# Kernel optimization log

Hardware: AMD Instinct MI355X
Metric: run time of the kernel (lower is better)

## Reference

```python
import jax, jax.numpy as jnp
import numpy as np

B, N, SEQ_LEN, OUT_LEN, E = 4, 5000, 128, 128, 80000
C_IN = SEQ_LEN + OUT_LEN  # DConv input is concat([X, H])


def setup_inputs() -> dict:
    key = jax.random.key(0)
    ks = jax.random.split(key, 9)
    scale = 0.02
    return {
        "x": jax.random.normal(ks[0], (B, N, SEQ_LEN), dtype=jnp.float32),
        "edge_index": jax.random.randint(ks[1], (2, E), 0, N, dtype=jnp.int32),
        "edge_weight": jax.random.uniform(ks[2], (E,), dtype=jnp.float32),
        "Wz": scale * jax.random.normal(ks[3], (2, 2, C_IN, OUT_LEN), dtype=jnp.float32),
        "bz": jnp.zeros((OUT_LEN,), jnp.float32),
        "Wr": scale * jax.random.normal(ks[4], (2, 2, C_IN, OUT_LEN), dtype=jnp.float32),
        "br": jnp.zeros((OUT_LEN,), jnp.float32),
        "Wh": scale * jax.random.normal(ks[5], (2, 2, C_IN, OUT_LEN), dtype=jnp.float32),
        "bh": jnp.zeros((OUT_LEN,), jnp.float32),
    }


def reference(x, edge_index, edge_weight, Wz, bz, Wr, br, Wh, bh):
    src, dst = edge_index[0], edge_index[1]
    # weighted out-/in-degrees and random-walk normalization (safe reciprocal)
    deg_out = jax.ops.segment_sum(edge_weight, src, num_segments=N)
    deg_in = jax.ops.segment_sum(edge_weight, dst, num_segments=N)
    dinv_out = jnp.where(deg_out > 0, 1.0 / deg_out, 0.0)
    dinv_in = jnp.where(deg_in > 0, 1.0 / deg_in, 0.0)
    coef_o = edge_weight * dinv_out[src]  # D_out^-1 W, per-edge
    coef_i = edge_weight * dinv_in[dst]   # D_in^-1 W^T, per-edge

    def dconv(Xc, W, b):
        # K=2 diffusion conv: identity terms + 1-hop forward + 1-hop reverse
        H = Xc @ (W[0, 0] + W[1, 0])
        Tx_o = jax.ops.segment_sum(coef_o[:, None] * Xc[src], dst, num_segments=N)
        Tx_i = jax.ops.segment_sum(coef_i[:, None] * Xc[dst], src, num_segments=N)
        return H + Tx_o @ W[0, 1] + Tx_i @ W[1, 1] + b

    def cell(X):  # X: [N, SEQ_LEN]; hidden state starts at zero each call
        H0 = jnp.zeros((N, OUT_LEN), X.dtype)
        Xc = jnp.concatenate([X, H0], axis=-1)
        Z = jax.nn.sigmoid(dconv(Xc, Wz, bz))
        R = jax.nn.sigmoid(dconv(Xc, Wr, br))
        Xc2 = jnp.concatenate([X, H0 * R], axis=-1)
        H_tilde = jnp.tanh(dconv(Xc2, Wh, bh))
        return Z * H0 + (1.0 - Z) * H_tilde

    return jax.vmap(cell)(x)  # [B, N, OUT_LEN]
```

## Files before the change

kernel.cpp:

```cpp
#include <hip/hip_runtime.h>
#include <math.h>

#define NN   5000
#define BB   4
#define SEQ  128
#define OUTC 128
#define EE   80000
#define KTOT 384
#define CTOT 256
#define MTOT (BB * NN)
#define MPAD 20096
#define CAP  64
#define EBLK 313
#define FBLK 384
#define XBLK 1250

typedef __attribute__((ext_vector_type(8))) short bf16x8;
typedef __attribute__((ext_vector_type(4))) float f32x4;

__device__ inline unsigned short f2bf(float f) {
    union { float f; unsigned u; } a; a.f = f;
    unsigned r = a.u + 0x7FFF + ((a.u >> 16) & 1);
    return (unsigned short)(r >> 16);
}

__global__ __launch_bounds__(256) void k_zero(float* __restrict__ z) {
    int i = blockIdx.x * blockDim.x + threadIdx.x;
    if (i < 5000) {
        f32x4 zz = {0.f, 0.f, 0.f, 0.f};
        *(f32x4*)&z[i * 4] = zz;
    }
}

__global__ __launch_bounds__(256) void k_bucket_fold(
        const int* __restrict__ ei, const float* __restrict__ ew,
        const float* __restrict__ x,
        const float* __restrict__ Wz, const float* __restrict__ bz,
        const float* __restrict__ Wh, const float* __restrict__ bh,
        float* deg_out, float* deg_in,
        unsigned* cnt_in, unsigned* cnt_out,
        int2* __restrict__ bin, int2* __restrict__ bout,
        unsigned short* __restrict__ WT, float* __restrict__ bcat2,
        unsigned short* __restrict__ xb16) {
    int bid = blockIdx.x;
    if (bid < EBLK) {
        int e = bid * 256 + threadIdx.x;
        if (e >= EE) return;
        int s = ei[e], d = ei[EE + e];
        float w = ew[e];
        atomicAdd(&deg_out[s], w);
        atomicAdd(&deg_in[d], w);
        unsigned p = atomicAdd(&cnt_in[d], 1u);
        if (p < CAP) bin[((size_t)d << 6) + p] = make_int2(s, __float_as_int(w));
        unsigned q = atomicAdd(&cnt_out[s], 1u);
        if (q < CAP) bout[((size_t)s << 6) + q] = make_int2(d, __float_as_int(w));
    } else if (bid < EBLK + FBLK) {
        int i = (bid - EBLK) * 256 + threadIdx.x;
        if (i < CTOT) bcat2[i] = (i & 1) ? bh[i >> 1] : bz[i >> 1];
        int cc = i / KTOT, k = i % KTOT;
        int gate = cc & 1, o = cc >> 1;
        const float* W = gate ? Wh : Wz;
        float v;
        if (k < 128)      v = W[(size_t)k * 128 + o] + W[(size_t)(512 + k) * 128 + o];
        else if (k < 256) v = W[(size_t)(256 + (k - 128)) * 128 + o];
        else              v = W[(size_t)(768 + (k - 256)) * 128 + o];
        WT[(size_t)cc * KTOT + k] = f2bf(v);
    } else {
        int j = (bid - EBLK - FBLK) * 256 + threadIdx.x;
        if (j < (BB * NN * SEQ) / 8) {
            const float4* xp = (const float4*)x;
            float4 v0 = xp[(size_t)j * 2], v1 = xp[(size_t)j * 2 + 1];
            uint4 pk;
            pk.x = (unsigned)f2bf(v0.x) | ((unsigned)f2bf(v0.y) << 16);
            pk.y = (unsigned)f2bf(v0.z) | ((unsigned)f2bf(v0.w) << 16);
            pk.z = (unsigned)f2bf(v1.x) | ((unsigned)f2bf(v1.y) << 16);
            pk.w = (unsigned)f2bf(v1.z) | ((unsigned)f2bf(v1.w) << 16);
            ((uint4*)xb16)[j] = pk;
        }
    }
}

#define ACC8(A, v, cf) {                                              \
    A[0] += (cf) * __uint_as_float((v).x << 16);                      \
    A[1] += (cf) * __uint_as_float((v).x & 0xFFFF0000u);              \
    A[2] += (cf) * __uint_as_float((v).y << 16);                      \
    A[3] += (cf) * __uint_as_float((v).y & 0xFFFF0000u);              \
    A[4] += (cf) * __uint_as_float((v).z << 16);                      \
    A[5] += (cf) * __uint_as_float((v).z & 0xFFFF0000u);              \
    A[6] += (cf) * __uint_as_float((v).w << 16);                      \
    A[7] += (cf) * __uint_as_float((v).w & 0xFFFF0000u); }

__global__ __launch_bounds__(256) void k_diffuse(
        const unsigned short* __restrict__ xb16,
        const float* __restrict__ deg_out, const float* __restrict__ deg_in,
        const unsigned* __restrict__ cnt_in, const unsigned* __restrict__ cnt_out,
        const int2* __restrict__ bin, const int2* __restrict__ bout,
        unsigned short* __restrict__ Inb) {
    __shared__ int2 sb[4][CAP + 4];
    int bid = blockIdx.x;
    int slot = bid & 7, pos = bid >> 3;
    int b = slot >> 1, half = slot & 1;
    int wv = threadIdx.x >> 6;
    int unit = pos * 4 + wv;
    int nl = unit >> 1;
    int list = unit & 1;
    int n = nl * 2 + half;
    int l = threadIdx.x & 63;
    int h = l >> 4, q = l & 15;
    const unsigned short* xb = xb16 + (size_t)b * NN * SEQ;

    const int2* bkt = list ? bout : bin;
    const float* dga = list ? deg_in : deg_out;
    int m = (int)min((list ? cnt_out : cnt_in)[n], (unsigned)CAP);
    if (l < m) {
        int2 e = bkt[((size_t)n << 6) + l];
        float dg = dga[e.x];
        float cf = dg > 0.f ? __int_as_float(e.y) / dg : 0.f;
        sb[wv][l] = make_int2(e.x, __float_as_int(cf));
    } else if (l < ((m + 3) & ~3)) {
        sb[wv][l] = make_int2(0, 0);
    }
    int me = (m + 3) & ~3;

    float a[8] = {0.f, 0.f, 0.f, 0.f, 0.f, 0.f, 0.f, 0.f};
    int j = 0;
    for (; j + 7 < me; j += 8) {
        int2 e0 = sb[wv][j + h], e1 = sb[wv][j + 4 + h];
        uint4 v0 = *(const uint4*)&xb[(size_t)e0.x * SEQ + 8 * q];
        uint4 v1 = *(const uint4*)&xb[(size_t)e1.x * SEQ + 8 * q];
        float c0 = __int_as_float(e0.y), c1 = __int_as_float(e1.y);
        ACC8(a, v0, c0);
        ACC8(a, v1, c1);
    }
    for (; j < me; j += 4) {
        int2 e0 = sb[wv][j + h];
        uint4 v0 = *(const uint4*)&xb[(size_t)e0.x * SEQ + 8 * q];
        float c0 = __int_as_float(e0.y);
        ACC8(a, v0, c0);
    }

#pragma unroll
    for (int r = 0; r < 8; ++r) {
        a[r] += __shfl_xor(a[r], 16);
        a[r] += __shfl_xor(a[r], 32);
    }

    if (h == 0) {
        unsigned short* rw = Inb + (size_t)(b * NN + n) * 256 + (list ? 128 : 0);
        uint4 pk;
        pk.x = (unsigned)f2bf(a[0]) | ((unsigned)f2bf(a[1]) << 16);
        pk.y = (unsigned)f2bf(a[2]) | ((unsigned)f2bf(a[3]) << 16);
        pk.z = (unsigned)f2bf(a[4]) | ((unsigned)f2bf(a[5]) << 16);
        pk.w = (unsigned)f2bf(a[6]) | ((unsigned)f2bf(a[7]) << 16);
        *(uint4*)&rw[8 * q] = pk;
    }
}

__global__ __launch_bounds__(512) void k_mm(
        const unsigned short* __restrict__ xb16,
        const unsigned short* __restrict__ Inb, const unsigned short* __restrict__ WT,
        const float* __restrict__ bcat2, float* __restrict__ out) {
    __shared__ unsigned short lA[3][4096];
    __shared__ unsigned short lB[3][4096];
    int t = threadIdx.x, w = t >> 6, l = t & 63;
    int lr = l & 15, lk = l >> 4;
    int n0 = blockIdx.x * 128;
    int c0 = blockIdx.y * 128;
    int wr = w >> 2, wc = w & 3;
    f32x4 acc[4][2] = {};

    int r = n0 + w * 16 + lr;
    int bidx = (r >= 15000) ? 3 : (r >= 10000) ? 2 : (r >= 5000) ? 1 : 0;
    const unsigned short* xrow = xb16 + ((size_t)bidx * NN + (r - bidx * NN)) * SEQ;
    const unsigned short* irow = Inb + (size_t)r * 256;
    const unsigned short* wrow = WT + (size_t)(c0 + w * 16 + lr) * KTOT;

#define STAGE(buf, k0)                                                            \
    {                                                                             \
        const unsigned short* sa = ((k0) < 128) ? (xrow + (k0) + lk * 8)          \
                                                : (irow + ((k0) - 128) + lk * 8); \
        __builtin_amdgcn_global_load_lds(                                         \
            (const __attribute__((address_space(1))) void*)sa,                    \
            (__attribute__((address_space(3))) void*)&lA[buf][w * 512], 16, 0, 0);\
        const unsigned short* sb = wrow + (k0) + lk * 8;                          \
        __builtin_amdgcn_global_load_lds(                                         \
            (const __attribute__((address_space(1))) void*)sb,                    \
            (__attribute__((address_space(3))) void*)&lB[buf][w * 512], 16, 0, 0);\
    }

    STAGE(0, 0);
    STAGE(1, 32);

#pragma unroll
    for (int ks = 0; ks < 12; ++ks) {
        if (ks < 11) asm volatile("s_waitcnt vmcnt(2)" ::: "memory");
        else         asm volatile("s_waitcnt vmcnt(0)" ::: "memory");
        __builtin_amdgcn_s_barrier();
        const int bf = ks % 3;
        bf16x8 a[4], bfr[2];
#pragma unroll
        for (int i = 0; i < 4; ++i) a[i] = *(const bf16x8*)&lA[bf][(wr * 4 + i) * 512 + l * 8];
#pragma unroll
        for (int jj = 0; jj < 2; ++jj) bfr[jj] = *(const bf16x8*)&lB[bf][(wc * 2 + jj) * 512 + l * 8];
#pragma unroll
        for (int i = 0; i < 4; ++i)
#pragma unroll
            for (int jj = 0; jj < 2; ++jj)
                acc[i][jj] = __builtin_amdgcn_mfma_f32_16x16x32_bf16(a[i], bfr[jj], acc[i][jj], 0, 0, 0);
        if (ks + 2 < 12) STAGE((ks + 2) % 3, (ks + 2) * 32);
    }
#undef STAGE

    int row_base = n0 + wr * 64;
    bool odd = (l & 1);
#pragma unroll
    for (int jj = 0; jj < 2; ++jj) {
        int cc = c0 + wc * 32 + jj * 16 + lr;
        float bias = bcat2[cc];
        int o = cc >> 1;
#pragma unroll
        for (int i = 0; i < 4; ++i) {
#pragma unroll
            for (int rr = 0; rr < 4; ++rr) {
                float v = acc[i][jj][rr] + bias;
                float ex = __expf(odd ? 2.f * v : v);
                float u = odd ? (1.f - 2.f / (ex + 1.f)) : (1.f / (1.f + ex));
                float g = __shfl_xor(u, 1);
                if (!odd) {
                    int row = row_base + i * 16 + lk * 4 + rr;
                    if (row < MTOT) out[(size_t)row * OUTC + o] = u * g;
                }
            }
        }
    }
}

extern "C" void kernel_launch(void* const* d_in, const int* in_sizes, int n_in,
                              void* d_out, int out_size, void* d_ws, size_t ws_size,
                              hipStream_t stream) {
    const float* x  = (const float*)d_in[0];
    const int*   ei = (const int*)d_in[1];
    const float* ew = (const float*)d_in[2];
    const float* Wz = (const float*)d_in[3];
    const float* bz = (const float*)d_in[4];
    const float* Wh = (const float*)d_in[7];
    const float* bh = (const float*)d_in[8];

    float* ws = (float*)d_ws;
    float*    deg_out = ws + 0;
    float*    deg_in  = ws + 5000;
    unsigned* cnt_in  = (unsigned*)(ws + 10000);
    unsigned* cnt_out = (unsigned*)(ws + 15000);
    float*    bcat2   = ws + 20000;
    unsigned short* WT = (unsigned short*)(ws + 20256);
    int2*     bin  = (int2*)(ws + 69408);
    int2*     bout = (int2*)(ws + 709408);
    unsigned short* xb16 = (unsigned short*)(ws + 1349408);
    unsigned short* Inb = (unsigned short*)(ws + 2629408);

    k_zero<<<20, 256, 0, stream>>>(ws);
    k_bucket_fold<<<EBLK + FBLK + XBLK, 256, 0, stream>>>(
        ei, ew, x, Wz, bz, Wh, bh, deg_out, deg_in, cnt_in, cnt_out,
        bin, bout, WT, bcat2, xb16);
    k_diffuse<<<2 * NN, 256, 0, stream>>>(xb16, deg_out, deg_in, cnt_in, cnt_out,
                                          bin, bout, Inb);
    dim3 g(MPAD / 128, 2);
    k_mm<<<g, 512, 0, stream>>>(xb16, Inb, WT, bcat2, (float*)d_out);
}
```

Baseline: 72.83 us.

## Fuse graph diffusion into GEMM kernel, keeping diffused features in shared memory

Merges the separate diffusion and matmul kernels into one kernel. Each 512-thread block first gathers the neighbor aggregates for 64 rows straight into LDS in MFMA fragment layout, then runs the bf16 MFMA GEMM over all 256 output columns. The X part and the weights are read directly from global memory into registers with double buffering, replacing the LDS staging pipeline. This removes a kernel launch and the global write and reread of the intermediate Inb buffer. The cost is a smaller row tile, a 32 KB LDS footprint that may limit occupancy, and weight reads that now come from global memory in every block without LDS sharing.

```diff
diff --git a/kernel.cpp b/kernel.cpp
--- a/kernel.cpp
+++ b/kernel.cpp
@@ -90,136 +90,136 @@
     A[6] += (cf) * __uint_as_float((v).w << 16);                      \
     A[7] += (cf) * __uint_as_float((v).w & 0xFFFF0000u); }
 
-__global__ __launch_bounds__(256) void k_diffuse(
+__global__ __launch_bounds__(512) void k_fused(
         const unsigned short* __restrict__ xb16,
         const float* __restrict__ deg_out, const float* __restrict__ deg_in,
         const unsigned* __restrict__ cnt_in, const unsigned* __restrict__ cnt_out,
         const int2* __restrict__ bin, const int2* __restrict__ bout,
-        unsigned short* __restrict__ Inb) {
-    __shared__ int2 sb[4][CAP + 4];
-    int bid = blockIdx.x;
-    int slot = bid & 7, pos = bid >> 3;
-    int b = slot >> 1, half = slot & 1;
-    int wv = threadIdx.x >> 6;
-    int unit = pos * 4 + wv;
-    int nl = unit >> 1;
-    int list = unit & 1;
-    int n = nl * 2 + half;
-    int l = threadIdx.x & 63;
-    int h = l >> 4, q = l & 15;
-    const unsigned short* xb = xb16 + (size_t)b * NN * SEQ;
-
-    const int2* bkt = list ? bout : bin;
-    const float* dga = list ? deg_in : deg_out;
-    int m = (int)min((list ? cnt_out : cnt_in)[n], (unsigned)CAP);
-    if (l < m) {
-        int2 e = bkt[((size_t)n << 6) + l];
-        float dg = dga[e.x];
-        float cf = dg > 0.f ? __int_as_float(e.y) / dg : 0.f;
-        sb[wv][l] = make_int2(e.x, __float_as_int(cf));
-    } else if (l < ((m + 3) & ~3)) {
-        sb[wv][l] = make_int2(0, 0);
-    }
-    int me = (m + 3) & ~3;
-
-    float a[8] = {0.f, 0.f, 0.f, 0.f, 0.f, 0.f, 0.f, 0.f};
-    int j = 0;
-    for (; j + 7 < me; j += 8) {
-        int2 e0 = sb[wv][j + h], e1 = sb[wv][j + 4 + h];
-        uint4 v0 = *(const uint4*)&xb[(size_t)e0.x * SEQ + 8 * q];
-        uint4 v1 = *(const uint4*)&xb[(size_t)e1.x * SEQ + 8 * q];
-        float c0 = __int_as_float(e0.y), c1 = __int_as_float(e1.y);
-        ACC8(a, v0, c0);
-        ACC8(a, v1, c1);
-    }
-    for (; j < me; j += 4) {
-        int2 e0 = sb[wv][j + h];
-        uint4 v0 = *(const uint4*)&xb[(size_t)e0.x * SEQ + 8 * q];
-        float c0 = __int_as_float(e0.y);
-        ACC8(a, v0, c0);
-    }
-
-#pragma unroll
-    for (int r = 0; r < 8; ++r) {
-        a[r] += __shfl_xor(a[r], 16);
-        a[r] += __shfl_xor(a[r], 32);
-    }
-
-    if (h == 0) {
-        unsigned short* rw = Inb + (size_t)(b * NN + n) * 256 + (list ? 128 : 0);
-        uint4 pk;
-        pk.x = (unsigned)f2bf(a[0]) | ((unsigned)f2bf(a[1]) << 16);
-        pk.y = (unsigned)f2bf(a[2]) | ((unsigned)f2bf(a[3]) << 16);
-        pk.z = (unsigned)f2bf(a[4]) | ((unsigned)f2bf(a[5]) << 16);
-        pk.w = (unsigned)f2bf(a[6]) | ((unsigned)f2bf(a[7]) << 16);
-        *(uint4*)&rw[8 * q] = pk;
-    }
-}
-
-__global__ __launch_bounds__(512) void k_mm(
-        const unsigned short* __restrict__ xb16,
-        const unsigned short* __restrict__ Inb, const unsigned short* __restrict__ WT,
-        const float* __restrict__ bcat2, float* __restrict__ out) {
-    __shared__ unsigned short lA[3][4096];
-    __shared__ unsigned short lB[3][4096];
+        const unsigned short* __restrict__ WT, const float* __restrict__ bcat2,
+        float* __restrict__ out) {
+    __shared__ unsigned short Tx[16384];
+    __shared__ int2 sb[8][CAP + 4];
     int t = threadIdx.x, w = t >> 6, l = t & 63;
+    int n0 = blockIdx.x * 64;
+
+    {
+        int h = l >> 4, q = l & 15;
+#pragma unroll 2
+        for (int it = 0; it < 16; ++it) {
+            int u = w + it * 8;
+            int row_local = u >> 1, list = u & 1;
+            int r = n0 + row_local;
+            int valid = (r < MTOT);
+            int b = (r >= 15000) ? 3 : (r >= 10000) ? 2 : (r >= 5000) ? 1 : 0;
+            int n = valid ? (r - b * NN) : 0;
+            if (!valid) b = 0;
+            const unsigned short* xb = xb16 + (size_t)b * NN * SEQ;
+            const int2* bkt = list ? bout : bin;
+            const float* dga = list ? deg_in : deg_out;
+            int m = valid ? (int)min((list ? cnt_out : cnt_in)[n], (unsigned)CAP) : 0;
+            if (l < m) {
+                int2 e = bkt[((size_t)n << 6) + l];
+                float dg = dga[e.x];
+                float cf = dg > 0.f ? __int_as_float(e.y) / dg : 0.f;
+                sb[w][l] = make_int2(e.x, __float_as_int(cf));
+            } else if (l < ((m + 3) & ~3)) {
+                sb[w][l] = make_int2(0, 0);
+            }
+            int me = (m + 3) & ~3;
+
+            float a[8] = {0.f, 0.f, 0.f, 0.f, 0.f, 0.f, 0.f, 0.f};
+            int j = 0;
+            for (; j + 7 < me; j += 8) {
+                int2 e0 = sb[w][j + h], e1 = sb[w][j + 4 + h];
+                uint4 v0 = *(const uint4*)&xb[(size_t)e0.x * SEQ + 8 * q];
+                uint4 v1 = *(const uint4*)&xb[(size_t)e1.x * SEQ + 8 * q];
+                float c0 = __int_as_float(e0.y), c1 = __int_as_float(e1.y);
+                ACC8(a, v0, c0);
+                ACC8(a, v1, c1);
+            }
+            for (; j < me; j += 4) {
+                int2 e0 = sb[w][j + h];
+                uint4 v0 = *(const uint4*)&xb[(size_t)e0.x * SEQ + 8 * q];
+                float c0 = __int_as_float(e0.y);
+                ACC8(a, v0, c0);
+            }
+#pragma unroll
+            for (int rr = 0; rr < 8; ++rr) {
+                a[rr] += __shfl_xor(a[rr], 16);
+                a[rr] += __shfl_xor(a[rr], 32);
+            }
+            if (h == 0) {
+                int jf = (list ? 4 : 0) + (q >> 2);
+                int rb = row_local >> 4, rl = row_local & 15;
+                uint4 pk;
+                pk.x = (unsigned)f2bf(a[0]) | ((unsigned)f2bf(a[1]) << 16);
+                pk.y = (unsigned)f2bf(a[2]) | ((unsigned)f2bf(a[3]) << 16);
+                pk.z = (unsigned)f2bf(a[4]) | ((unsigned)f2bf(a[5]) << 16);
+                pk.w = (unsigned)f2bf(a[6]) | ((unsigned)f2bf(a[7]) << 16);
+                *(uint4*)&Tx[(rb * 8 + jf) * 512 + rl * 8 + (q & 3) * 128] = pk;
+            }
+        }
+    }
+    __syncthreads();
+
     int lr = l & 15, lk = l >> 4;
-    int n0 = blockIdx.x * 128;
-    int c0 = blockIdx.y * 128;
     int wr = w >> 2, wc = w & 3;
-    f32x4 acc[4][2] = {};
-
-    int r = n0 + w * 16 + lr;
-    int bidx = (r >= 15000) ? 3 : (r >= 10000) ? 2 : (r >= 5000) ? 1 : 0;
-    const unsigned short* xrow = xb16 + ((size_t)bidx * NN + (r - bidx * NN)) * SEQ;
-    const unsigned short* irow = Inb + (size_t)r * 256;
-    const unsigned short* wrow = WT + (size_t)(c0 + w * 16 + lr) * KTOT;
-
-#define STAGE(buf, k0)                                                            \
-    {                                                                             \
-        const unsigned short* sa = ((k0) < 128) ? (xrow + (k0) + lk * 8)          \
-                                                : (irow + ((k0) - 128) + lk * 8); \
-        __builtin_amdgcn_global_load_lds(                                         \
-            (const __attribute__((address_space(1))) void*)sa,                    \
-            (__attribute__((address_space(3))) void*)&lA[buf][w * 512], 16, 0, 0);\
-        const unsigned short* sb = wrow + (k0) + lk * 8;                          \
-        __builtin_amdgcn_global_load_lds(                                         \
-            (const __attribute__((address_space(1))) void*)sb,                    \
-            (__attribute__((address_space(3))) void*)&lB[buf][w * 512], 16, 0, 0);\
-    }
-
-    STAGE(0, 0);
-    STAGE(1, 32);
-
+    f32x4 acc[2][4] = {};
+
+    const unsigned short* wp[4];
+#pragma unroll
+    for (int jj = 0; jj < 4; ++jj)
+        wp[jj] = WT + (size_t)((wc * 4 + jj) * 16 + lr) * KTOT + lk * 8;
+
+    const unsigned short* xp[2];
+#pragma unroll
+    for (int i = 0; i < 2; ++i) {
+        int r = n0 + (wr * 2 + i) * 16 + lr;
+        if (r >= MTOT) r = 0;
+        int b = (r >= 15000) ? 3 : (r >= 10000) ? 2 : (r >= 5000) ? 1 : 0;
+        xp[i] = xb16 + ((size_t)b * NN + (r - b * NN)) * SEQ + lk * 8;
+    }
+
+    bf16x8 ar[2][2], br[2][4];
+#define LOADK(buf, ks) {                                                          \
+        if ((ks) < 8) {                                                           \
+            _Pragma("unroll")                                                     \
+            for (int i = 0; i < 2; ++i)                                           \
+                ar[buf][i] = *(const bf16x8*)&Tx[((wr * 2 + i) * 8 + (ks)) * 512 + l * 8]; \
+            _Pragma("unroll")                                                     \
+            for (int jj = 0; jj < 4; ++jj)                                        \
+                br[buf][jj] = *(const bf16x8*)(wp[jj] + 128 + 32 * (ks));         \
+        } else {                                                                  \
+            _Pragma("unroll")                                                     \
+            for (int i = 0; i < 2; ++i)                                           \
+                ar[buf][i] = *(const bf16x8*)(xp[i] + 32 * ((ks) - 8));           \
+            _Pragma("unroll")                                                     \
+            for (int jj = 0; jj < 4; ++jj)                                        \
+                br[buf][jj] = *(const bf16x8*)(wp[jj] + 32 * ((ks) - 8));         \
+        } }
+
+    LOADK(0, 0);
 #pragma unroll
     for (int ks = 0; ks < 12; ++ks) {
-        if (ks < 11) asm volatile("s_waitcnt vmcnt(2)" ::: "memory");
-        else         asm volatile("s_waitcnt vmcnt(0)" ::: "memory");
-        __builtin_amdgcn_s_barrier();
-        const int bf = ks % 3;
-        bf16x8 a[4], bfr[2];
-#pragma unroll
-        for (int i = 0; i < 4; ++i) a[i] = *(const bf16x8*)&lA[bf][(wr * 4 + i) * 512 + l * 8];
-#pragma unroll
-        for (int jj = 0; jj < 2; ++jj) bfr[jj] = *(const bf16x8*)&lB[bf][(wc * 2 + jj) * 512 + l * 8];
-#pragma unroll
-        for (int i = 0; i < 4; ++i)
-#pragma unroll
-            for (int jj = 0; jj < 2; ++jj)
-                acc[i][jj] = __builtin_amdgcn_mfma_f32_16x16x32_bf16(a[i], bfr[jj], acc[i][jj], 0, 0, 0);
-        if (ks + 2 < 12) STAGE((ks + 2) % 3, (ks + 2) * 32);
-    }
-#undef STAGE
-
-    int row_base = n0 + wr * 64;
+        if (ks + 1 < 12) LOADK((ks + 1) & 1, ks + 1);
+#pragma unroll
+        for (int i = 0; i < 2; ++i)
+#pragma unroll
+            for (int jj = 0; jj < 4; ++jj)
+                acc[i][jj] = __builtin_amdgcn_mfma_f32_16x16x32_bf16(
+                    ar[ks & 1][i], br[ks & 1][jj], acc[i][jj], 0, 0, 0);
+    }
+#undef LOADK
+
+    int row_base = n0 + wr * 32;
     bool odd = (l & 1);
 #pragma unroll
-    for (int jj = 0; jj < 2; ++jj) {
-        int cc = c0 + wc * 32 + jj * 16 + lr;
+    for (int jj = 0; jj < 4; ++jj) {
+        int cc = wc * 64 + jj * 16 + lr;
         float bias = bcat2[cc];
         int o = cc >> 1;
 #pragma unroll
-        for (int i = 0; i < 4; ++i) {
+        for (int i = 0; i < 2; ++i) {
 #pragma unroll
             for (int rr = 0; rr < 4; ++rr) {
                 float v = acc[i][jj][rr] + bias;
@@ -256,14 +256,11 @@
     int2*     bin  = (int2*)(ws + 69408);
     int2*     bout = (int2*)(ws + 709408);
     unsigned short* xb16 = (unsigned short*)(ws + 1349408);
-    unsigned short* Inb = (unsigned short*)(ws + 2629408);
 
     k_zero<<<20, 256, 0, stream>>>(ws);
     k_bucket_fold<<<EBLK + FBLK + XBLK, 256, 0, stream>>>(
         ei, ew, x, Wz, bz, Wh, bh, deg_out, deg_in, cnt_in, cnt_out,
         bin, bout, WT, bcat2, xb16);
-    k_diffuse<<<2 * NN, 256, 0, stream>>>(xb16, deg_out, deg_in, cnt_in, cnt_out,
-                                          bin, bout, Inb);
-    dim3 g(MPAD / 128, 2);
-    k_mm<<<g, 512, 0, stream>>>(xb16, Inb, WT, bcat2, (float*)d_out);
-}
+    k_fused<<<MPAD / 64, 512, 0, stream>>>(xb16, deg_out, deg_in, cnt_in, cnt_out,
+                                           bin, bout, WT, bcat2, (float*)d_out);
+}
```

Result: slower. 106.1 us (+45.6%).

## Pre-scale node features by inverse degree instead of per-edge degree lookups

Applied to the files above, without the earlier changes.

Drops the float atomic degree accumulation from the edge-bucketing kernel. A new per-node kernel computes each node's degrees by reducing its bucketed edge weights, converts x to bf16, and writes two extra bf16 copies of x pre-multiplied by the inverse out- and in-degree. The diffusion kernel then uses the raw edge weight as its coefficient and gathers from the pre-scaled copy, removing the dependent deg[e.x] gather and division per edge. The cost is one more kernel launch and about twice the bf16 feature writes, plus degrees that silently ignore edges beyond the 64-per-node bucket cap.

```diff
diff --git a/kernel.cpp b/kernel.cpp
--- a/kernel.cpp
+++ b/kernel.cpp
@@ -13,7 +13,6 @@
 #define CAP  64
 #define EBLK 313
 #define FBLK 384
-#define XBLK 1250
 
 typedef __attribute__((ext_vector_type(8))) short bf16x8;
 typedef __attribute__((ext_vector_type(4))) float f32x4;
@@ -24,37 +23,32 @@
     return (unsigned short)(r >> 16);
 }
 
-__global__ __launch_bounds__(256) void k_zero(float* __restrict__ z) {
+__global__ __launch_bounds__(256) void k_zero(unsigned* __restrict__ z) {
     int i = blockIdx.x * blockDim.x + threadIdx.x;
-    if (i < 5000) {
-        f32x4 zz = {0.f, 0.f, 0.f, 0.f};
-        *(f32x4*)&z[i * 4] = zz;
+    if (i < 2500) {
+        uint4 zz = {0u, 0u, 0u, 0u};
+        ((uint4*)z)[i] = zz;
     }
 }
 
 __global__ __launch_bounds__(256) void k_bucket_fold(
         const int* __restrict__ ei, const float* __restrict__ ew,
-        const float* __restrict__ x,
         const float* __restrict__ Wz, const float* __restrict__ bz,
         const float* __restrict__ Wh, const float* __restrict__ bh,
-        float* deg_out, float* deg_in,
         unsigned* cnt_in, unsigned* cnt_out,
         int2* __restrict__ bin, int2* __restrict__ bout,
-        unsigned short* __restrict__ WT, float* __restrict__ bcat2,
-        unsigned short* __restrict__ xb16) {
+        unsigned short* __restrict__ WT, float* __restrict__ bcat2) {
     int bid = blockIdx.x;
     if (bid < EBLK) {
         int e = bid * 256 + threadIdx.x;
         if (e >= EE) return;
         int s = ei[e], d = ei[EE + e];
         float w = ew[e];
-        atomicAdd(&deg_out[s], w);
-        atomicAdd(&deg_in[d], w);
         unsigned p = atomicAdd(&cnt_in[d], 1u);
         if (p < CAP) bin[((size_t)d << 6) + p] = make_int2(s, __float_as_int(w));
         unsigned q = atomicAdd(&cnt_out[s], 1u);
         if (q < CAP) bout[((size_t)s << 6) + q] = make_int2(d, __float_as_int(w));
-    } else if (bid < EBLK + FBLK) {
+    } else {
         int i = (bid - EBLK) * 256 + threadIdx.x;
         if (i < CTOT) bcat2[i] = (i & 1) ? bh[i >> 1] : bz[i >> 1];
         int cc = i / KTOT, k = i % KTOT;
@@ -65,18 +59,37 @@
         else if (k < 256) v = W[(size_t)(256 + (k - 128)) * 128 + o];
         else              v = W[(size_t)(768 + (k - 256)) * 128 + o];
         WT[(size_t)cc * KTOT + k] = f2bf(v);
-    } else {
-        int j = (bid - EBLK - FBLK) * 256 + threadIdx.x;
-        if (j < (BB * NN * SEQ) / 8) {
-            const float4* xp = (const float4*)x;
-            float4 v0 = xp[(size_t)j * 2], v1 = xp[(size_t)j * 2 + 1];
-            uint4 pk;
-            pk.x = (unsigned)f2bf(v0.x) | ((unsigned)f2bf(v0.y) << 16);
-            pk.y = (unsigned)f2bf(v0.z) | ((unsigned)f2bf(v0.w) << 16);
-            pk.z = (unsigned)f2bf(v1.x) | ((unsigned)f2bf(v1.y) << 16);
-            pk.w = (unsigned)f2bf(v1.z) | ((unsigned)f2bf(v1.w) << 16);
-            ((uint4*)xb16)[j] = pk;
-        }
+    }
+}
+
+__global__ __launch_bounds__(256) void k_norm(
+        const float* __restrict__ x,
+        const unsigned* __restrict__ cnt_in, const unsigned* __restrict__ cnt_out,
+        const int2* __restrict__ bin, const int2* __restrict__ bout,
+        unsigned short* __restrict__ xb16,
+        unsigned short* __restrict__ xn_o, unsigned short* __restrict__ xn_i) {
+    int wv = threadIdx.x >> 6, l = threadIdx.x & 63;
+    int n = blockIdx.x * 4 + wv;
+    if (n >= NN) return;
+    int mi = (int)min(cnt_in[n], (unsigned)CAP);
+    int mo = (int)min(cnt_out[n], (unsigned)CAP);
+    float wi = 0.f, wo = 0.f;
+    if (l < mi) wi = __int_as_float(bin[((size_t)n << 6) + l].y);
+    if (l < mo) wo = __int_as_float(bout[((size_t)n << 6) + l].y);
+#pragma unroll
+    for (int s = 1; s < 64; s <<= 1) {
+        wi += __shfl_xor(wi, s);
+        wo += __shfl_xor(wo, s);
+    }
+    float dio = wo > 0.f ? 1.f / wo : 0.f;
+    float dii = wi > 0.f ? 1.f / wi : 0.f;
+#pragma unroll
+    for (int b = 0; b < BB; ++b) {
+        size_t off = ((size_t)b * NN + n) * SEQ + 2 * l;
+        float2 xv = *(const float2*)&x[off];
+        *(unsigned*)&xb16[off] = (unsigned)f2bf(xv.x) | ((unsigned)f2bf(xv.y) << 16);
+        *(unsigned*)&xn_o[off] = (unsigned)f2bf(xv.x * dio) | ((unsigned)f2bf(xv.y * dio) << 16);
+        *(unsigned*)&xn_i[off] = (unsigned)f2bf(xv.x * dii) | ((unsigned)f2bf(xv.y * dii) << 16);
     }
 }
 
@@ -91,8 +104,7 @@
     A[7] += (cf) * __uint_as_float((v).w & 0xFFFF0000u); }
 
 __global__ __launch_bounds__(256) void k_diffuse(
-        const unsigned short* __restrict__ xb16,
-        const float* __restrict__ deg_out, const float* __restrict__ deg_in,
+        const unsigned short* __restrict__ xn_o, const unsigned short* __restrict__ xn_i,
         const unsigned* __restrict__ cnt_in, const unsigned* __restrict__ cnt_out,
         const int2* __restrict__ bin, const int2* __restrict__ bout,
         unsigned short* __restrict__ Inb) {
@@ -107,16 +119,12 @@
     int n = nl * 2 + half;
     int l = threadIdx.x & 63;
     int h = l >> 4, q = l & 15;
-    const unsigned short* xb = xb16 + (size_t)b * NN * SEQ;
+    const unsigned short* xs = (list ? xn_i : xn_o) + (size_t)b * NN * SEQ;
 
     const int2* bkt = list ? bout : bin;
-    const float* dga = list ? deg_in : deg_out;
     int m = (int)min((list ? cnt_out : cnt_in)[n], (unsigned)CAP);
     if (l < m) {
-        int2 e = bkt[((size_t)n << 6) + l];
-        float dg = dga[e.x];
-        float cf = dg > 0.f ? __int_as_float(e.y) / dg : 0.f;
-        sb[wv][l] = make_int2(e.x, __float_as_int(cf));
+        sb[wv][l] = bkt[((size_t)n << 6) + l];
     } else if (l < ((m + 3) & ~3)) {
         sb[wv][l] = make_int2(0, 0);
     }
@@ -126,15 +134,15 @@
     int j = 0;
     for (; j + 7 < me; j += 8) {
         int2 e0 = sb[wv][j + h], e1 = sb[wv][j + 4 + h];
-        uint4 v0 = *(const uint4*)&xb[(size_t)e0.x * SEQ + 8 * q];
-        uint4 v1 = *(const uint4*)&xb[(size_t)e1.x * SEQ + 8 * q];
+        uint4 v0 = *(const uint4*)&xs[(size_t)e0.x * SEQ + 8 * q];
+        uint4 v1 = *(const uint4*)&xs[(size_t)e1.x * SEQ + 8 * q];
         float c0 = __int_as_float(e0.y), c1 = __int_as_float(e1.y);
         ACC8(a, v0, c0);
         ACC8(a, v1, c1);
     }
     for (; j < me; j += 4) {
         int2 e0 = sb[wv][j + h];
-        uint4 v0 = *(const uint4*)&xb[(size_t)e0.x * SEQ + 8 * q];
+        uint4 v0 = *(const uint4*)&xs[(size_t)e0.x * SEQ + 8 * q];
         float c0 = __int_as_float(e0.y);
         ACC8(a, v0, c0);
     }
@@ -247,23 +255,22 @@
     const float* bh = (const float*)d_in[8];
 
     float* ws = (float*)d_ws;
-    float*    deg_out = ws + 0;
-    float*    deg_in  = ws + 5000;
-    unsigned* cnt_in  = (unsigned*)(ws + 10000);
-    unsigned* cnt_out = (unsigned*)(ws + 15000);
-    float*    bcat2   = ws + 20000;
-    unsigned short* WT = (unsigned short*)(ws + 20256);
-    int2*     bin  = (int2*)(ws + 69408);
-    int2*     bout = (int2*)(ws + 709408);
-    unsigned short* xb16 = (unsigned short*)(ws + 1349408);
-    unsigned short* Inb = (unsigned short*)(ws + 2629408);
-
-    k_zero<<<20, 256, 0, stream>>>(ws);
-    k_bucket_fold<<<EBLK + FBLK + XBLK, 256, 0, stream>>>(
-        ei, ew, x, Wz, bz, Wh, bh, deg_out, deg_in, cnt_in, cnt_out,
-        bin, bout, WT, bcat2, xb16);
-    k_diffuse<<<2 * NN, 256, 0, stream>>>(xb16, deg_out, deg_in, cnt_in, cnt_out,
-                                          bin, bout, Inb);
+    unsigned* cnt_in  = (unsigned*)(ws + 0);
+    unsigned* cnt_out = (unsigned*)(ws + 5000);
+    float*    bcat2   = ws + 10000;
+    unsigned short* WT = (unsigned short*)(ws + 10256);
+    int2*     bin  = (int2*)(ws + 59408);
+    int2*     bout = (int2*)(ws + 699408);
+    unsigned short* xb16 = (unsigned short*)(ws + 1339408);
+    unsigned short* xn_o = (unsigned short*)(ws + 2619408);
+    unsigned short* xn_i = (unsigned short*)(ws + 3899408);
+    unsigned short* Inb  = (unsigned short*)(ws + 5179408);
+
+    k_zero<<<10, 256, 0, stream>>>((unsigned*)ws);
+    k_bucket_fold<<<EBLK + FBLK, 256, 0, stream>>>(
+        ei, ew, Wz, bz, Wh, bh, cnt_in, cnt_out, bin, bout, WT, bcat2);
+    k_norm<<<1250, 256, 0, stream>>>(x, cnt_in, cnt_out, bin, bout, xb16, xn_o, xn_i);
+    k_diffuse<<<2 * NN, 256, 0, stream>>>(xn_o, xn_i, cnt_in, cnt_out, bin, bout, Inb);
     dim3 g(MPAD / 128, 2);
     k_mm<<<g, 512, 0, stream>>>(xb16, Inb, WT, bcat2, (float*)d_out);
 }
```

After: 68.80 us. 5.5% less time.
